# Optimization experiments

Hardware: AMD Instinct MI355X
Metric: run time of the kernel (lower is better)

## Reference

```python
import jax, jax.numpy as jnp
import numpy as np

N_USER = 100000
N_ITEM = 100000
E = 1600000
B = 16384
D = 128
LAYERS = [128, 128]
NEG_SLOPE = 0.2
EPS = 1e-12


def _l2norm(x):
    # F.normalize(x, dim=1, p=2): x / max(||x||, eps)
    n = jnp.sqrt(jnp.sum(x * x, axis=1, keepdims=True))
    return x / jnp.maximum(n, EPS)


def _sage_layer(h, src, dst, W_self, W_neigh, b):
    # DGL SAGEConv('mean'): mean-aggregate neighbor feats, then
    # fc_self(h) + fc_neigh(h_neigh) + bias
    msg = h[src]                                   # [E, D_in] gather
    agg = jax.ops.segment_sum(msg, dst, num_segments=h.shape[0])
    deg = jax.ops.segment_sum(jnp.ones((src.shape[0],), h.dtype), dst,
                              num_segments=h.shape[0])
    h_neigh = agg / jnp.maximum(deg, 1.0)[:, None]  # zero in-degree -> 0
    out = h @ W_self + h_neigh @ W_neigh + b
    return jax.nn.leaky_relu(out, NEG_SLOPE)


def setup_inputs() -> dict:
    key = jax.random.key(0)
    ks = jax.random.split(key, 20)
    inp = {}
    inp["src"] = jax.random.randint(ks[0], (E,), 0, N_USER)
    inp["dst"] = jax.random.randint(ks[1], (E,), 0, N_USER)
    inp["users"] = jax.random.randint(ks[2], (B,), 0, N_USER)
    inp["pos_items"] = jax.random.randint(ks[3], (B,), 0, N_ITEM)
    inp["neg_items"] = jax.random.randint(ks[4], (B,), 0, N_ITEM)
    inp["user_feat"] = jax.random.normal(ks[5], (N_USER, D), jnp.float32) * 0.05
    inp["item_feat"] = jax.random.normal(ks[6], (N_ITEM, D), jnp.float32) * 0.05
    dims = [D] + LAYERS
    i = 7
    for l in range(len(LAYERS)):
        di, do = dims[l], dims[l + 1]
        s = 1.0 / np.sqrt(di)
        inp[f"Wu_self{l}"] = jax.random.normal(ks[i], (di, do), jnp.float32) * s; i += 1
        inp[f"Wu_neigh{l}"] = jax.random.normal(ks[i], (di, do), jnp.float32) * s; i += 1
        inp[f"bu{l}"] = jnp.zeros((do,), jnp.float32)
        inp[f"Wi{l}"] = jax.random.normal(ks[i], (di, do), jnp.float32) * s; i += 1
        inp[f"bi{l}"] = jnp.zeros((do,), jnp.float32)
    return inp


def reference(src, dst, users, pos_items, neg_items, user_feat, item_feat,
              Wu_self0, Wu_neigh0, bu0, Wi0, bi0,
              Wu_self1, Wu_neigh1, bu1, Wi1, bi1):
    user_params = [(Wu_self0, Wu_neigh0, bu0), (Wu_self1, Wu_neigh1, bu1)]
    item_params = [(Wi0, bi0), (Wi1, bi1)]

    h_u = user_feat
    user_embeds = [h_u]
    for (Ws, Wn, b) in user_params:
        h_u = _sage_layer(h_u, src, dst, Ws, Wn, b)
        h_u = _l2norm(h_u)  # dropout p=0 -> identity
        user_embeds.append(h_u)

    h_i = item_feat
    item_embeds = [h_i]
    for (W, b) in item_params:
        h_i = jax.nn.leaky_relu(h_i @ W + b, NEG_SLOPE)
        h_i = _l2norm(h_i)
        item_embeds.append(h_i)

    user_embd = jnp.concatenate(user_embeds, axis=1)   # [N_user, 3*D]
    item_embd = jnp.concatenate(item_embeds, axis=1)   # [N_item, 3*D]

    return (user_embd[users], item_embd[pos_items], item_embd[neg_items])
```

## Files before the change

kernel.cpp:

```cpp
#include <hip/hip_runtime.h>

#define NU 100000
#define NI 100000
#define NE 1600000
#define BB 16384
#define DD 128

static constexpr int SCAN_CHUNK = 2048;
static constexpr int SCAN_NBLK  = (NU + SCAN_CHUNK - 1) / SCAN_CHUNK;
static constexpr int USER_TILES = NU / 16;

static constexpr int NXCD   = 8;
static constexpr int DRANGE = NU / NXCD;
static constexpr int K_CH   = 32;
static constexpr int CHUNK4 = NE / 4 / K_CH;
static constexpr int HIST_BLKS = NXCD * K_CH;
static constexpr int PACK_BLKS = 48;
static constexpr int CVT_UNIT  = 2048;
static constexpr int CVT_TOT   = NU * 32;
static constexpr int CVT_BLKS  = (CVT_TOT + CVT_UNIT - 1) / CVT_UNIT;

static constexpr size_t OFF_DEG      = 0;
static constexpr size_t OFF_ROWSTART = 400128;
static constexpr size_t OFF_BSUM     = 1200384;
static constexpr size_t OFF_EDGESRC  = 1200640;
static constexpr size_t OFF_H1       = 7600640;
static constexpr size_t OFF_WFRAG    = 58800640;


typedef __bf16 bf16x8 __attribute__((ext_vector_type(8)));
typedef float f32x4 __attribute__((ext_vector_type(4)));
typedef unsigned int u32x4 __attribute__((ext_vector_type(4)));

union frag_u {
    u32x4 u;
    bf16x8 b;
    unsigned short us[8];
};

__device__ __forceinline__ unsigned short f2bf(float f) {
    unsigned u = __float_as_uint(f);
    u = (u + 0x7fffu + ((u >> 16) & 1u)) >> 16;
    return (unsigned short)u;
}

__device__ __forceinline__ unsigned pack_bf16_pair(float a, float b) {
    return (unsigned)f2bf(a) | ((unsigned)f2bf(b) << 16);
}

__device__ __forceinline__ float2 unpack_bf16_pair(unsigned u) {
    float2 r;
    r.x = __uint_as_float(u << 16);
    r.y = __uint_as_float(u & 0xffff0000u);
    return r;
}

__device__ __forceinline__ f32x4 mfma16(bf16x8 a, bf16x8 b, f32x4 c) {
    return __builtin_amdgcn_mfma_f32_16x16x32_bf16(a, b, c, 0, 0, 0);
}

__device__ __forceinline__ bf16x8 bfrag(const u32x4* __restrict__ wf, int idx) {
    frag_u f;
    f.u = wf[idx];
    return f.b;
}

__device__ __forceinline__ void make_afrag_hilo(const float* rowp, int kb,
                                                bf16x8* hi, bf16x8* lo) {
    float4 v0 = *(const float4*)(rowp + kb);
    float4 v1 = *(const float4*)(rowp + kb + 4);
    float vv[8] = {v0.x, v0.y, v0.z, v0.w, v1.x, v1.y, v1.z, v1.w};
    frag_u h, l;
    #pragma unroll
    for (int e = 0; e < 8; ++e) {
        unsigned short hb = f2bf(vv[e]);
        h.us[e] = hb;
        float hf = __uint_as_float(((unsigned)hb) << 16);
        l.us[e] = f2bf(vv[e] - hf);
    }
    *hi = h.b;
    *lo = l.b;
}

__global__ __launch_bounds__(256) void mega_prep(
    const int* __restrict__ dst, int* __restrict__ hist,
    const float* __restrict__ uf, unsigned* __restrict__ ubf,
    const float* __restrict__ Ws0, const float* __restrict__ Wn0,
    const float* __restrict__ Ws1, const float* __restrict__ Wn1,
    const float* __restrict__ Wi0, const float* __restrict__ Wi1,
    u32x4* __restrict__ wfrag) {
    __shared__ int h[DRANGE];
    int t = threadIdx.x;
    if (blockIdx.x < HIST_BLKS) {
        int r = blockIdx.x & (NXCD - 1);
        int k = blockIdx.x >> 3;
        for (int j = t; j < DRANGE; j += 256) h[j] = 0;
        __syncthreads();
        int lo = r * DRANGE;
        const int4* d4 = (const int4*)dst + (size_t)k * CHUNK4;
        for (int i = t; i < CHUNK4; i += 256) {
            int4 d = d4[i];
            if ((unsigned)(d.x - lo) < (unsigned)DRANGE) atomicAdd(&h[d.x - lo], 1);
            if ((unsigned)(d.y - lo) < (unsigned)DRANGE) atomicAdd(&h[d.y - lo], 1);
            if ((unsigned)(d.z - lo) < (unsigned)DRANGE) atomicAdd(&h[d.z - lo], 1);
            if ((unsigned)(d.w - lo) < (unsigned)DRANGE) atomicAdd(&h[d.w - lo], 1);
        }
        __syncthreads();
        int* hb = hist + (size_t)(r * K_CH + k) * DRANGE;
        for (int j = t; j < DRANGE; j += 256) hb[j] = h[j];
    } else if (blockIdx.x < HIST_BLKS + PACK_BLKS) {
        int i = (blockIdx.x - HIST_BLKS) * 256 + t;
        const float* tab[6] = {Ws0, Wn0, Ws1, Wn1, Wi0, Wi1};
        int matg = i >> 11;
        int j = (i >> 8) & 7, kk = (i >> 6) & 3, ln = i & 63;
        const float* W = tab[matg];
        int n = j * 16 + (ln & 15);
        int kb = kk * 32 + (ln >> 4) * 8;
        unsigned short u[8];
        #pragma unroll
        for (int e = 0; e < 8; ++e) u[e] = f2bf(W[(size_t)(kb + e) * DD + n]);
        u32x4 w;
        w[0] = u[0] | ((unsigned)u[1] << 16);
        w[1] = u[2] | ((unsigned)u[3] << 16);
        w[2] = u[4] | ((unsigned)u[5] << 16);
        w[3] = u[6] | ((unsigned)u[7] << 16);
        wfrag[i] = w;
    } else {
        int bid2 = blockIdx.x - HIST_BLKS - PACK_BLKS;
        const float4* uf4 = (const float4*)uf;
        uint2* ub2 = (uint2*)ubf;
        #pragma unroll
        for (int it = 0; it < 8; ++it) {
            int idx = bid2 * CVT_UNIT + it * 256 + t;
            if (idx < CVT_TOT) {
                float4 v = uf4[idx];
                uint2 o;
                o.x = pack_bf16_pair(v.x, v.y);
                o.y = pack_bf16_pair(v.z, v.w);
                ub2[idx] = o;
            }
        }
    }
}

__global__ __launch_bounds__(256) void deg_reduce(const int* __restrict__ hist,
                                                  int* __restrict__ deg) {
    int d = blockIdx.x * 256 + threadIdx.x;
    if (d >= NU) return;
    int r = d / DRANGE, j = d - r * DRANGE;
    const int* hb = hist + (size_t)r * K_CH * DRANGE + j;
    int s = 0;
    #pragma unroll
    for (int k = 0; k < K_CH; ++k) s += hb[(size_t)k * DRANGE];
    deg[d] = s;
}

__global__ __launch_bounds__(256) void scan1_kernel(const int* __restrict__ deg,
                                                    int* __restrict__ bsum) {
    __shared__ int sh[256];
    int t = threadIdx.x;
    int base = blockIdx.x * SCAN_CHUNK + t * 8;
    int s = 0;
    #pragma unroll
    for (int j = 0; j < 8; ++j) {
        int idx = base + j;
        s += (idx < NU) ? deg[idx] : 0;
    }
    sh[t] = s;
    __syncthreads();
    for (int off = 128; off > 0; off >>= 1) {
        if (t < off) sh[t] += sh[t + off];
        __syncthreads();
    }
    if (t == 0) bsum[blockIdx.x] = sh[0];
}

__global__ void scan2_kernel(int* __restrict__ bsum) {
    if (threadIdx.x == 0) {
        int acc = 0;
        for (int i = 0; i < SCAN_NBLK; ++i) {
            int v = bsum[i];
            bsum[i] = acc;
            acc += v;
        }
    }
}

__global__ __launch_bounds__(256) void scan3_kernel(const int* __restrict__ deg,
                                                    const int* __restrict__ bsum,
                                                    int* __restrict__ row_start) {
    __shared__ int sh[256];
    int t = threadIdx.x;
    int base = blockIdx.x * SCAN_CHUNK + t * 8;
    int v[8];
    int s = 0;
    #pragma unroll
    for (int j = 0; j < 8; ++j) {
        int idx = base + j;
        v[j] = (idx < NU) ? deg[idx] : 0;
        s += v[j];
    }
    sh[t] = s;
    __syncthreads();
    for (int off = 1; off < 256; off <<= 1) {
        int val = sh[t];
        int add = (t >= off) ? sh[t - off] : 0;
        __syncthreads();
        sh[t] = val + add;
        __syncthreads();
    }
    int excl = sh[t] - s + bsum[blockIdx.x];
    #pragma unroll
    for (int j = 0; j < 8; ++j) {
        int idx = base + j;
        if (idx < NU) row_start[idx] = excl;
        excl += v[j];
    }
}

__global__ __launch_bounds__(256) void base_kernel(const int* __restrict__ row_start,
                                                   int* __restrict__ hist) {
    int d = blockIdx.x * 256 + threadIdx.x;
    if (d >= NU) return;
    int r = d / DRANGE, j = d - r * DRANGE;
    int* hb = hist + (size_t)r * K_CH * DRANGE + j;
    int acc = row_start[d];
    #pragma unroll
    for (int k = 0; k < K_CH; ++k) {
        int c = hb[(size_t)k * DRANGE];
        hb[(size_t)k * DRANGE] = acc;
        acc += c;
    }
}

__global__ __launch_bounds__(256) void fill2(const int* __restrict__ src,
                                             const int* __restrict__ dst,
                                             const int* __restrict__ base,
                                             int* __restrict__ edge_src) {
    __shared__ int cur[DRANGE];
    int r = blockIdx.x & (NXCD - 1);
    int k = blockIdx.x >> 3;
    int t = threadIdx.x;
    const int* bb = base + (size_t)(r * K_CH + k) * DRANGE;
    for (int j = t; j < DRANGE; j += 256) cur[j] = bb[j];
    __syncthreads();
    int lo = r * DRANGE;
    const int4* d4 = (const int4*)dst + (size_t)k * CHUNK4;
    const int4* s4 = (const int4*)src + (size_t)k * CHUNK4;
    for (int i = t; i < CHUNK4; i += 256) {
        int4 d = d4[i];
        int4 s = s4[i];
        if ((unsigned)(d.x - lo) < (unsigned)DRANGE) edge_src[atomicAdd(&cur[d.x - lo], 1)] = s.x;
        if ((unsigned)(d.y - lo) < (unsigned)DRANGE) edge_src[atomicAdd(&cur[d.y - lo], 1)] = s.y;
        if ((unsigned)(d.z - lo) < (unsigned)DRANGE) edge_src[atomicAdd(&cur[d.z - lo], 1)] = s.z;
        if ((unsigned)(d.w - lo) < (unsigned)DRANGE) edge_src[atomicAdd(&cur[d.w - lo], 1)] = s.w;
    }
}

__global__ __launch_bounds__(256) void agg_kernel(const unsigned* __restrict__ ubf,
                                                  const int* __restrict__ row_start,
                                                  const int* __restrict__ deg,
                                                  const int* __restrict__ edge_src,
                                                  unsigned* __restrict__ hn) {
    int wid = blockIdx.x * 4 + (threadIdx.x >> 6);
    int lane = threadIdx.x & 63;
    if (wid >= NU) return;
    int st = row_start[wid];
    int dg = deg[wid];
    int lanelet = lane & 15;
    int eslot = lane >> 4;
    float acc[8] = {0.f, 0.f, 0.f, 0.f, 0.f, 0.f, 0.f, 0.f};
    const unsigned* colp = ubf + (lanelet << 2);
    for (int base = 0; base < dg; base += 64) {
        int n = min(dg - base, 64);
        int myidx = (lane < n) ? edge_src[st + base + lane] : 0;
        int e = 0;
        #pragma unroll 2
        for (; e + 4 <= n; e += 4) {
            int s = __shfl(myidx, e + eslot, 64);
            u32x4 v = *(const u32x4*)(colp + (size_t)s * 64);
            #pragma unroll
            for (int k = 0; k < 4; ++k) {
                float2 f = unpack_bf16_pair(v[k]);
                acc[2 * k] += f.x;
                acc[2 * k + 1] += f.y;
            }
        }
        int rem = n - e;
        int s = __shfl(myidx, min(e + eslot, 63), 64);
        if (eslot < rem) {
            u32x4 v = *(const u32x4*)(colp + (size_t)s * 64);
            #pragma unroll
            for (int k = 0; k < 4; ++k) {
                float2 f = unpack_bf16_pair(v[k]);
                acc[2 * k] += f.x;
                acc[2 * k + 1] += f.y;
            }
        }
    }
    #pragma unroll
    for (int k = 0; k < 8; ++k) {
        acc[k] += __shfl_xor(acc[k], 16, 64);
        acc[k] += __shfl_xor(acc[k], 32, 64);
    }
    float inv = 1.0f / fmaxf((float)dg, 1.0f);
    if (eslot == 0) {
        u32x4 o;
        o[0] = pack_bf16_pair(acc[0] * inv, acc[1] * inv);
        o[1] = pack_bf16_pair(acc[2] * inv, acc[3] * inv);
        o[2] = pack_bf16_pair(acc[4] * inv, acc[5] * inv);
        o[3] = pack_bf16_pair(acc[6] * inv, acc[7] * inv);
        *(u32x4*)(hn + (size_t)wid * 64 + (lanelet << 2)) = o;
    }
}

__global__ __launch_bounds__(256) void user_mm_mfma(
    const float* __restrict__ hself, const unsigned short* __restrict__ hn,
    const u32x4* __restrict__ wf, const float* __restrict__ bias,
    float* __restrict__ out) {
    int t = threadIdx.x;
    int lane = t & 63;
    int tile = blockIdx.x * 4 + (t >> 6);
    if (tile >= USER_TILES) return;
    int gbase = tile * 16;
    int m = lane & 15, q = lane >> 4;
    const float* selfp = hself + (size_t)(gbase + m) * DD;
    const unsigned short* neighp = hn + (size_t)(gbase + m) * DD;
    bf16x8 as_hi[4], as_lo[4], an[4];
    #pragma unroll
    for (int kk = 0; kk < 4; ++kk) {
        int kb = kk * 32 + q * 8;
        make_afrag_hilo(selfp, kb, &as_hi[kk], &as_lo[kk]);
        frag_u f;
        f.u = *(const u32x4*)(neighp + kb);
        an[kk] = f.b;
    }
    f32x4 acc[8];
    f32x4 zero = {0.f, 0.f, 0.f, 0.f};
    #pragma unroll
    for (int j = 0; j < 8; ++j) acc[j] = zero;
    #pragma unroll 2
    for (int j = 0; j < 8; ++j) {
        #pragma unroll
        for (int kk = 0; kk < 4; ++kk) {
            bf16x8 bs = bfrag(wf, (j * 4 + kk) * 64 + lane);
            acc[j] = mfma16(as_hi[kk], bs, acc[j]);
            acc[j] = mfma16(as_lo[kk], bs, acc[j]);
            bf16x8 bn = bfrag(wf, 2048 + (j * 4 + kk) * 64 + lane);
            acc[j] = mfma16(an[kk], bn, acc[j]);
        }
    }
    float ss[4] = {0.f, 0.f, 0.f, 0.f};
    #pragma unroll
    for (int j = 0; j < 8; ++j) {
        float bj = bias[j * 16 + m];
        #pragma unroll
        for (int r = 0; r < 4; ++r) {
            float x = acc[j][r] + bj;
            x = x > 0.f ? x : 0.2f * x;
            acc[j][r] = x;
            ss[r] += x * x;
        }
    }
    #pragma unroll
    for (int r = 0; r < 4; ++r) {
        float s = ss[r];
        s += __shfl_xor(s, 1, 64);
        s += __shfl_xor(s, 2, 64);
        s += __shfl_xor(s, 4, 64);
        s += __shfl_xor(s, 8, 64);
        ss[r] = 1.0f / fmaxf(sqrtf(s), 1e-12f);
    }
    #pragma unroll
    for (int j = 0; j < 8; ++j)
        #pragma unroll
        for (int r = 0; r < 4; ++r)
            out[(size_t)(gbase + q * 4 + r) * DD + j * 16 + m] = acc[j][r] * ss[r];
}

__global__ __launch_bounds__(256) void tail_fuse(
    const float* __restrict__ ufeat, const float* __restrict__ h1,
    const int* __restrict__ users, const int* __restrict__ row_start,
    const int* __restrict__ deg, const int* __restrict__ edge_src,
    const float* __restrict__ ifeat, const int* __restrict__ pos,
    const int* __restrict__ neg, const u32x4* __restrict__ wf_u,
    const u32x4* __restrict__ wf_i, const float* __restrict__ bu1,
    const float* __restrict__ bi0, const float* __restrict__ bi1,
    float* __restrict__ out) {
    __shared__ float sc[16 * 132];
    __shared__ float ssp[16 * 4];
    int t = threadIdx.x;
    int lane = t & 63, wave = t >> 6;
    int m = lane & 15, q = lane >> 4;
    f32x4 zero = {0.f, 0.f, 0.f, 0.f};

    if (blockIdx.x < 1024) {
        int gb = blockIdx.x * 16;
        int L = lane & 31;
        int eslot = lane >> 5;
        const float* hl = h1 + 4 * L;
        #pragma unroll
        for (int rr = 0; rr < 4; ++rr) {
            int r = wave * 4 + rr;
            int u = users[gb + r];
            int st = row_start[u], dg = deg[u];
            float ax = 0.f, ay = 0.f, az = 0.f, aw = 0.f;
            for (int base = 0; base < dg; base += 64) {
                int n = min(dg - base, 64);
                int myidx = (lane < n) ? edge_src[st + base + lane] : 0;
                int e = 0;
                #pragma unroll 4
                for (; e + 2 <= n; e += 2) {
                    int s = __shfl(myidx, e + eslot, 64);
                    float4 v = *(const float4*)(hl + (size_t)s * DD);
                    ax += v.x; ay += v.y; az += v.z; aw += v.w;
                }
                if (e < n) {
                    int s = __shfl(myidx, e, 64);
                    if (eslot == 0) {
                        float4 v = *(const float4*)(hl + (size_t)s * DD);
                        ax += v.x; ay += v.y; az += v.z; aw += v.w;
                    }
                }
            }
            ax += __shfl_xor(ax, 32, 64);
            ay += __shfl_xor(ay, 32, 64);
            az += __shfl_xor(az, 32, 64);
            aw += __shfl_xor(aw, 32, 64);
            float inv = 1.0f / fmaxf((float)dg, 1.0f);
            if (eslot == 0) {
                float4 o = {ax * inv, ay * inv, az * inv, aw * inv};
                *(float4*)(sc + r * 132 + 4 * L) = o;
            }
            float* orow = out + (size_t)(gb + r) * 384;
            ((float2*)orow)[lane] = ((const float2*)(ufeat + (size_t)u * DD))[lane];
            ((float2*)orow)[64 + lane] = ((const float2*)(h1 + (size_t)u * DD))[lane];
        }
        __syncthreads();
        int j0 = wave * 2;
        int um = users[gb + m];
        const float* selfp = h1 + (size_t)um * DD;
        bf16x8 sh[4], sl[4], nh[4], nl[4];
        #pragma unroll
        for (int kk = 0; kk < 4; ++kk) {
            int kb = kk * 32 + q * 8;
            make_afrag_hilo(selfp, kb, &sh[kk], &sl[kk]);
            make_afrag_hilo(sc + m * 132, kb, &nh[kk], &nl[kk]);
        }
        f32x4 a0 = zero, a1 = zero;
        #pragma unroll
        for (int kk = 0; kk < 4; ++kk) {
            bf16x8 b0 = bfrag(wf_u, (j0 * 4 + kk) * 64 + lane);
            a0 = mfma16(sh[kk], b0, a0);
            a0 = mfma16(sl[kk], b0, a0);
            bf16x8 n0 = bfrag(wf_u, 2048 + (j0 * 4 + kk) * 64 + lane);
            a0 = mfma16(nh[kk], n0, a0);
            a0 = mfma16(nl[kk], n0, a0);
            bf16x8 b1 = bfrag(wf_u, ((j0 + 1) * 4 + kk) * 64 + lane);
            a1 = mfma16(sh[kk], b1, a1);
            a1 = mfma16(sl[kk], b1, a1);
            bf16x8 n1 = bfrag(wf_u, 2048 + ((j0 + 1) * 4 + kk) * 64 + lane);
            a1 = mfma16(nh[kk], n1, a1);
            a1 = mfma16(nl[kk], n1, a1);
        }
        float bj0 = bu1[j0 * 16 + m], bj1 = bu1[(j0 + 1) * 16 + m];
        float ss[4];
        #pragma unroll
        for (int r = 0; r < 4; ++r) {
            float x0 = a0[r] + bj0; x0 = x0 > 0.f ? x0 : 0.2f * x0; a0[r] = x0;
            float x1 = a1[r] + bj1; x1 = x1 > 0.f ? x1 : 0.2f * x1; a1[r] = x1;
            float s = x0 * x0 + x1 * x1;
            s += __shfl_xor(s, 1, 64);
            s += __shfl_xor(s, 2, 64);
            s += __shfl_xor(s, 4, 64);
            s += __shfl_xor(s, 8, 64);
            ss[r] = s;
        }
        if (m == 0) {
            #pragma unroll
            for (int r = 0; r < 4; ++r) ssp[(q * 4 + r) * 4 + wave] = ss[r];
        }
        __syncthreads();
        #pragma unroll
        for (int r = 0; r < 4; ++r) {
            int row = q * 4 + r;
            float tot = ssp[row * 4] + ssp[row * 4 + 1] + ssp[row * 4 + 2] + ssp[row * 4 + 3];
            float inv = 1.0f / fmaxf(sqrtf(tot), 1e-12f);
            out[(size_t)(gb + row) * 384 + 256 + j0 * 16 + m] = a0[r] * inv;
            out[(size_t)(gb + row) * 384 + 256 + (j0 + 1) * 16 + m] = a1[r] * inv;
        }
        return;
    }

    int tile = blockIdx.x - 1024;
    int gb = tile * 16;
    int j0 = wave * 2;
    int rowm = gb + m;
    int idxm = (rowm < BB) ? pos[rowm] : neg[rowm - BB];
    const float* rowp = ifeat + (size_t)idxm * DD;
    bf16x8 ahi[4], alo[4];
    #pragma unroll
    for (int kk = 0; kk < 4; ++kk)
        make_afrag_hilo(rowp, kk * 32 + q * 8, &ahi[kk], &alo[kk]);
    f32x4 a0 = zero, a1 = zero;
    #pragma unroll
    for (int kk = 0; kk < 4; ++kk) {
        bf16x8 b0 = bfrag(wf_i, (j0 * 4 + kk) * 64 + lane);
        a0 = mfma16(ahi[kk], b0, a0);
        a0 = mfma16(alo[kk], b0, a0);
        bf16x8 b1 = bfrag(wf_i, ((j0 + 1) * 4 + kk) * 64 + lane);
        a1 = mfma16(ahi[kk], b1, a1);
        a1 = mfma16(alo[kk], b1, a1);
    }
    {
        float bj0 = bi0[j0 * 16 + m], bj1 = bi0[(j0 + 1) * 16 + m];
        float ss[4];
        #pragma unroll
        for (int r = 0; r < 4; ++r) {
            float x0 = a0[r] + bj0; x0 = x0 > 0.f ? x0 : 0.2f * x0; a0[r] = x0;
            float x1 = a1[r] + bj1; x1 = x1 > 0.f ? x1 : 0.2f * x1; a1[r] = x1;
            float s = x0 * x0 + x1 * x1;
            s += __shfl_xor(s, 1, 64);
            s += __shfl_xor(s, 2, 64);
            s += __shfl_xor(s, 4, 64);
            s += __shfl_xor(s, 8, 64);
            ss[r] = s;
        }
        if (m == 0) {
            #pragma unroll
            for (int r = 0; r < 4; ++r) ssp[(q * 4 + r) * 4 + wave] = ss[r];
        }
        __syncthreads();
        #pragma unroll
        for (int r = 0; r < 4; ++r) {
            int row = q * 4 + r;
            float tot = ssp[row * 4] + ssp[row * 4 + 1] + ssp[row * 4 + 2] + ssp[row * 4 + 3];
            float inv = 1.0f / fmaxf(sqrtf(tot), 1e-12f);
            sc[row * 132 + j0 * 16 + m] = a0[r] * inv;
            sc[row * 132 + (j0 + 1) * 16 + m] = a1[r] * inv;
        }
        __syncthreads();
    }
    #pragma unroll
    for (int rr = 0; rr < 4; ++rr) {
        int r = wave * 4 + rr;
        int row = gb + r;
        int idx = (row < BB) ? pos[row] : neg[row - BB];
        float* orow = out + (size_t)(BB + row) * 384;
        ((float2*)orow)[lane] = ((const float2*)(ifeat + (size_t)idx * DD))[lane];
        float2 r1v;
        r1v.x = sc[r * 132 + 2 * lane];
        r1v.y = sc[r * 132 + 2 * lane + 1];
        ((float2*)orow)[64 + lane] = r1v;
    }
    bf16x8 chi[4], clo[4];
    #pragma unroll
    for (int kk = 0; kk < 4; ++kk)
        make_afrag_hilo(sc + m * 132, kk * 32 + q * 8, &chi[kk], &clo[kk]);
    a0 = zero; a1 = zero;
    #pragma unroll
    for (int kk = 0; kk < 4; ++kk) {
        bf16x8 b0 = bfrag(wf_i, 2048 + (j0 * 4 + kk) * 64 + lane);
        a0 = mfma16(chi[kk], b0, a0);
        a0 = mfma16(clo[kk], b0, a0);
        bf16x8 b1 = bfrag(wf_i, 2048 + ((j0 + 1) * 4 + kk) * 64 + lane);
        a1 = mfma16(chi[kk], b1, a1);
        a1 = mfma16(clo[kk], b1, a1);
    }
    {
        float bj0 = bi1[j0 * 16 + m], bj1 = bi1[(j0 + 1) * 16 + m];
        float ss[4];
        #pragma unroll
        for (int r = 0; r < 4; ++r) {
            float x0 = a0[r] + bj0; x0 = x0 > 0.f ? x0 : 0.2f * x0; a0[r] = x0;
            float x1 = a1[r] + bj1; x1 = x1 > 0.f ? x1 : 0.2f * x1; a1[r] = x1;
            float s = x0 * x0 + x1 * x1;
            s += __shfl_xor(s, 1, 64);
            s += __shfl_xor(s, 2, 64);
            s += __shfl_xor(s, 4, 64);
            s += __shfl_xor(s, 8, 64);
            ss[r] = s;
        }
        __syncthreads();
        if (m == 0) {
            #pragma unroll
            for (int r = 0; r < 4; ++r) ssp[(q * 4 + r) * 4 + wave] = ss[r];
        }
        __syncthreads();
        #pragma unroll
        for (int r = 0; r < 4; ++r) {
            int row = q * 4 + r;
            float tot = ssp[row * 4] + ssp[row * 4 + 1] + ssp[row * 4 + 2] + ssp[row * 4 + 3];
            float inv = 1.0f / fmaxf(sqrtf(tot), 1e-12f);
            out[(size_t)(BB + gb + row) * 384 + 256 + j0 * 16 + m] = a0[r] * inv;
            out[(size_t)(BB + gb + row) * 384 + 256 + (j0 + 1) * 16 + m] = a1[r] * inv;
        }
    }
}

extern "C" void kernel_launch(void* const* d_in, const int* in_sizes, int n_in,
                              void* d_out, int out_size, void* d_ws, size_t ws_size,
                              hipStream_t stream) {
    const int* src = (const int*)d_in[0];
    const int* dst = (const int*)d_in[1];
    const int* users = (const int*)d_in[2];
    const int* pos = (const int*)d_in[3];
    const int* neg = (const int*)d_in[4];
    const float* ufeat = (const float*)d_in[5];
    const float* ifeat = (const float*)d_in[6];
    const float* Ws0 = (const float*)d_in[7];
    const float* Wn0 = (const float*)d_in[8];
    const float* bu0 = (const float*)d_in[9];
    const float* Wi0 = (const float*)d_in[10];
    const float* bi0 = (const float*)d_in[11];
    const float* Ws1 = (const float*)d_in[12];
    const float* Wn1 = (const float*)d_in[13];
    const float* bu1 = (const float*)d_in[14];
    const float* Wi1 = (const float*)d_in[15];
    const float* bi1 = (const float*)d_in[16];
    float* out = (float*)d_out;

    char* ws = (char*)d_ws;
    int* deg = (int*)(ws + OFF_DEG);
    int* row_start = (int*)(ws + OFF_ROWSTART);
    int* bsum = (int*)(ws + OFF_BSUM);
    int* edge_src = (int*)(ws + OFF_EDGESRC);
    float* h1 = (float*)(ws + OFF_H1);
    u32x4* wfrag = (u32x4*)(ws + OFF_WFRAG);

    unsigned* ubf = (unsigned*)d_out;
    unsigned* hn = (unsigned*)((char*)d_out + (size_t)NU * DD * 2);
    int* hist = (int*)((char*)d_out + (size_t)NU * DD * 4);
    const unsigned short* hn_us = (const unsigned short*)hn;

    mega_prep<<<HIST_BLKS + PACK_BLKS + CVT_BLKS, 256, 0, stream>>>(
        dst, hist, ufeat, ubf, Ws0, Wn0, Ws1, Wn1, Wi0, Wi1, wfrag);
    deg_reduce<<<(NU + 255) / 256, 256, 0, stream>>>(hist, deg);
    scan1_kernel<<<SCAN_NBLK, 256, 0, stream>>>(deg, bsum);
    scan2_kernel<<<1, 64, 0, stream>>>(bsum);
    scan3_kernel<<<SCAN_NBLK, 256, 0, stream>>>(deg, bsum, row_start);
    base_kernel<<<(NU + 255) / 256, 256, 0, stream>>>(row_start, hist);
    fill2<<<HIST_BLKS, 256, 0, stream>>>(src, dst, hist, edge_src);
    agg_kernel<<<(NU + 3) / 4, 256, 0, stream>>>(ubf, row_start, deg, edge_src, hn);
    user_mm_mfma<<<(USER_TILES + 3) / 4, 256, 0, stream>>>(ufeat, hn_us, wfrag, bu0, h1);
    tail_fuse<<<1024 + 2048, 256, 0, stream>>>(ufeat, h1, users, row_start, deg, edge_src,
                                               ifeat, pos, neg, wfrag + 4096, wfrag + 8192,
                                               bu1, bi0, bi1, out);
}
```

Measured before the change: 440.1 us.

## Interleave item MLP blocks with neighbor aggregation and split user tail kernel

Merges the layer-0 neighbor aggregation and the item-tower MLP into one launch, interleaving item tiles among aggregation blocks so the compute-bound item work overlaps the gather-bound aggregation. The user tail is split into its own kernel. The bf16 conversion covers only the first 98304 rows, and gathers from higher rows read fp32 features directly, so the convert loop needs no bounds check. The aggregation result is written into the h1 buffer with a 256-element stride and then overwritten in place by user_mm_mfma, removing the separate hn buffer. This adds a divergent branch in the gather loop and depends on ordering: each user_mm tile reads its hn rows before writing h1 over them.

Measured after the change: 486.3 us. +10.5%, slower.

```diff
diff --git a/kernel.cpp b/kernel.cpp
--- a/kernel.cpp
+++ b/kernel.cpp
@@ -16,9 +16,14 @@
 static constexpr int CHUNK4 = NE / 4 / K_CH;
 static constexpr int HIST_BLKS = NXCD * K_CH;
 static constexpr int PACK_BLKS = 48;
+static constexpr int UBF_ROWS  = 98304;
 static constexpr int CVT_UNIT  = 2048;
-static constexpr int CVT_TOT   = NU * 32;
-static constexpr int CVT_BLKS  = (CVT_TOT + CVT_UNIT - 1) / CVT_UNIT;
+static constexpr int CVT_TOT   = UBF_ROWS * 32;
+static constexpr int CVT_BLKS  = CVT_TOT / CVT_UNIT;
+
+static constexpr int NITEM  = 2048;
+static constexpr int AGG_BLKS = NU / 4;
+static constexpr int AI_BLKS  = AGG_BLKS + NITEM;
 
 static constexpr size_t OFF_DEG      = 0;
 static constexpr size_t OFF_ROWSTART = 400128;
@@ -132,13 +137,11 @@
         #pragma unroll
         for (int it = 0; it < 8; ++it) {
             int idx = bid2 * CVT_UNIT + it * 256 + t;
-            if (idx < CVT_TOT) {
-                float4 v = uf4[idx];
-                uint2 o;
-                o.x = pack_bf16_pair(v.x, v.y);
-                o.y = pack_bf16_pair(v.z, v.w);
-                ub2[idx] = o;
-            }
+            float4 v = uf4[idx];
+            uint2 o;
+            o.x = pack_bf16_pair(v.x, v.y);
+            o.y = pack_bf16_pair(v.z, v.w);
+            ub2[idx] = o;
         }
     }
 }
@@ -257,244 +260,97 @@
     }
 }
 
-__global__ __launch_bounds__(256) void agg_kernel(const unsigned* __restrict__ ubf,
-                                                  const int* __restrict__ row_start,
-                                                  const int* __restrict__ deg,
-                                                  const int* __restrict__ edge_src,
-                                                  unsigned* __restrict__ hn) {
-    int wid = blockIdx.x * 4 + (threadIdx.x >> 6);
-    int lane = threadIdx.x & 63;
-    if (wid >= NU) return;
-    int st = row_start[wid];
-    int dg = deg[wid];
-    int lanelet = lane & 15;
-    int eslot = lane >> 4;
-    float acc[8] = {0.f, 0.f, 0.f, 0.f, 0.f, 0.f, 0.f, 0.f};
-    const unsigned* colp = ubf + (lanelet << 2);
-    for (int base = 0; base < dg; base += 64) {
-        int n = min(dg - base, 64);
-        int myidx = (lane < n) ? edge_src[st + base + lane] : 0;
-        int e = 0;
-        #pragma unroll 2
-        for (; e + 4 <= n; e += 4) {
-            int s = __shfl(myidx, e + eslot, 64);
-            u32x4 v = *(const u32x4*)(colp + (size_t)s * 64);
-            #pragma unroll
-            for (int k = 0; k < 4; ++k) {
-                float2 f = unpack_bf16_pair(v[k]);
-                acc[2 * k] += f.x;
-                acc[2 * k + 1] += f.y;
-            }
-        }
-        int rem = n - e;
-        int s = __shfl(myidx, min(e + eslot, 63), 64);
-        if (eslot < rem) {
-            u32x4 v = *(const u32x4*)(colp + (size_t)s * 64);
-            #pragma unroll
-            for (int k = 0; k < 4; ++k) {
-                float2 f = unpack_bf16_pair(v[k]);
-                acc[2 * k] += f.x;
-                acc[2 * k + 1] += f.y;
-            }
-        }
-    }
-    #pragma unroll
-    for (int k = 0; k < 8; ++k) {
-        acc[k] += __shfl_xor(acc[k], 16, 64);
-        acc[k] += __shfl_xor(acc[k], 32, 64);
-    }
-    float inv = 1.0f / fmaxf((float)dg, 1.0f);
-    if (eslot == 0) {
-        u32x4 o;
-        o[0] = pack_bf16_pair(acc[0] * inv, acc[1] * inv);
-        o[1] = pack_bf16_pair(acc[2] * inv, acc[3] * inv);
-        o[2] = pack_bf16_pair(acc[4] * inv, acc[5] * inv);
-        o[3] = pack_bf16_pair(acc[6] * inv, acc[7] * inv);
-        *(u32x4*)(hn + (size_t)wid * 64 + (lanelet << 2)) = o;
-    }
-}
-
-__global__ __launch_bounds__(256) void user_mm_mfma(
-    const float* __restrict__ hself, const unsigned short* __restrict__ hn,
-    const u32x4* __restrict__ wf, const float* __restrict__ bias,
-    float* __restrict__ out) {
-    int t = threadIdx.x;
-    int lane = t & 63;
-    int tile = blockIdx.x * 4 + (t >> 6);
-    if (tile >= USER_TILES) return;
-    int gbase = tile * 16;
-    int m = lane & 15, q = lane >> 4;
-    const float* selfp = hself + (size_t)(gbase + m) * DD;
-    const unsigned short* neighp = hn + (size_t)(gbase + m) * DD;
-    bf16x8 as_hi[4], as_lo[4], an[4];
-    #pragma unroll
-    for (int kk = 0; kk < 4; ++kk) {
-        int kb = kk * 32 + q * 8;
-        make_afrag_hilo(selfp, kb, &as_hi[kk], &as_lo[kk]);
-        frag_u f;
-        f.u = *(const u32x4*)(neighp + kb);
-        an[kk] = f.b;
-    }
-    f32x4 acc[8];
-    f32x4 zero = {0.f, 0.f, 0.f, 0.f};
-    #pragma unroll
-    for (int j = 0; j < 8; ++j) acc[j] = zero;
-    #pragma unroll 2
-    for (int j = 0; j < 8; ++j) {
-        #pragma unroll
-        for (int kk = 0; kk < 4; ++kk) {
-            bf16x8 bs = bfrag(wf, (j * 4 + kk) * 64 + lane);
-            acc[j] = mfma16(as_hi[kk], bs, acc[j]);
-            acc[j] = mfma16(as_lo[kk], bs, acc[j]);
-            bf16x8 bn = bfrag(wf, 2048 + (j * 4 + kk) * 64 + lane);
-            acc[j] = mfma16(an[kk], bn, acc[j]);
-        }
-    }
-    float ss[4] = {0.f, 0.f, 0.f, 0.f};
-    #pragma unroll
-    for (int j = 0; j < 8; ++j) {
-        float bj = bias[j * 16 + m];
-        #pragma unroll
-        for (int r = 0; r < 4; ++r) {
-            float x = acc[j][r] + bj;
-            x = x > 0.f ? x : 0.2f * x;
-            acc[j][r] = x;
-            ss[r] += x * x;
-        }
-    }
-    #pragma unroll
-    for (int r = 0; r < 4; ++r) {
-        float s = ss[r];
-        s += __shfl_xor(s, 1, 64);
-        s += __shfl_xor(s, 2, 64);
-        s += __shfl_xor(s, 4, 64);
-        s += __shfl_xor(s, 8, 64);
-        ss[r] = 1.0f / fmaxf(sqrtf(s), 1e-12f);
-    }
-    #pragma unroll
-    for (int j = 0; j < 8; ++j)
-        #pragma unroll
-        for (int r = 0; r < 4; ++r)
-            out[(size_t)(gbase + q * 4 + r) * DD + j * 16 + m] = acc[j][r] * ss[r];
-}
-
-__global__ __launch_bounds__(256) void tail_fuse(
-    const float* __restrict__ ufeat, const float* __restrict__ h1,
-    const int* __restrict__ users, const int* __restrict__ row_start,
-    const int* __restrict__ deg, const int* __restrict__ edge_src,
+__global__ __launch_bounds__(256) void agg_item_fuse(
+    const unsigned* __restrict__ ubf, const float* __restrict__ ufeat,
+    const int* __restrict__ row_start, const int* __restrict__ deg,
+    const int* __restrict__ edge_src, float* __restrict__ h1,
     const float* __restrict__ ifeat, const int* __restrict__ pos,
-    const int* __restrict__ neg, const u32x4* __restrict__ wf_u,
-    const u32x4* __restrict__ wf_i, const float* __restrict__ bu1,
+    const int* __restrict__ neg, const u32x4* __restrict__ wf_i,
     const float* __restrict__ bi0, const float* __restrict__ bi1,
     float* __restrict__ out) {
     __shared__ float sc[16 * 132];
     __shared__ float ssp[16 * 4];
+    int bid = blockIdx.x;
     int t = threadIdx.x;
     int lane = t & 63, wave = t >> 6;
-    int m = lane & 15, q = lane >> 4;
-    f32x4 zero = {0.f, 0.f, 0.f, 0.f};
-
-    if (blockIdx.x < 1024) {
-        int gb = blockIdx.x * 16;
-        int L = lane & 31;
-        int eslot = lane >> 5;
-        const float* hl = h1 + 4 * L;
-        #pragma unroll
-        for (int rr = 0; rr < 4; ++rr) {
-            int r = wave * 4 + rr;
-            int u = users[gb + r];
-            int st = row_start[u], dg = deg[u];
-            float ax = 0.f, ay = 0.f, az = 0.f, aw = 0.f;
-            for (int base = 0; base < dg; base += 64) {
-                int n = min(dg - base, 64);
-                int myidx = (lane < n) ? edge_src[st + base + lane] : 0;
-                int e = 0;
-                #pragma unroll 4
-                for (; e + 2 <= n; e += 2) {
-                    int s = __shfl(myidx, e + eslot, 64);
-                    float4 v = *(const float4*)(hl + (size_t)s * DD);
-                    ax += v.x; ay += v.y; az += v.z; aw += v.w;
-                }
-                if (e < n) {
-                    int s = __shfl(myidx, e, 64);
-                    if (eslot == 0) {
-                        float4 v = *(const float4*)(hl + (size_t)s * DD);
-                        ax += v.x; ay += v.y; az += v.z; aw += v.w;
+    bool is_item = (bid % 13 == 6) && (bid / 13 < NITEM);
+
+    if (!is_item) {
+        int agg_bid = bid - min(NITEM, (bid + 6) / 13);
+        int wid = agg_bid * 4 + wave;
+        int st = row_start[wid];
+        int dg = deg[wid];
+        int lanelet = lane & 15;
+        int eslot = lane >> 4;
+        float acc[8] = {0.f, 0.f, 0.f, 0.f, 0.f, 0.f, 0.f, 0.f};
+        const unsigned* colp = ubf + (lanelet << 2);
+        const float* fcol = ufeat + (lanelet << 3);
+        for (int base = 0; base < dg; base += 64) {
+            int n = min(dg - base, 64);
+            int myidx = (lane < n) ? edge_src[st + base + lane] : 0;
+            int e = 0;
+            #pragma unroll 2
+            for (; e + 4 <= n; e += 4) {
+                int s = __shfl(myidx, e + eslot, 64);
+                if (s < UBF_ROWS) {
+                    u32x4 v = *(const u32x4*)(colp + (size_t)s * 64);
+                    #pragma unroll
+                    for (int k = 0; k < 4; ++k) {
+                        float2 f = unpack_bf16_pair(v[k]);
+                        acc[2 * k] += f.x;
+                        acc[2 * k + 1] += f.y;
                     }
+                } else {
+                    const float* fp = fcol + (size_t)s * DD;
+                    float4 a = *(const float4*)fp;
+                    float4 b = *(const float4*)(fp + 4);
+                    acc[0] += a.x; acc[1] += a.y; acc[2] += a.z; acc[3] += a.w;
+                    acc[4] += b.x; acc[5] += b.y; acc[6] += b.z; acc[7] += b.w;
                 }
             }
-            ax += __shfl_xor(ax, 32, 64);
-            ay += __shfl_xor(ay, 32, 64);
-            az += __shfl_xor(az, 32, 64);
-            aw += __shfl_xor(aw, 32, 64);
-            float inv = 1.0f / fmaxf((float)dg, 1.0f);
-            if (eslot == 0) {
-                float4 o = {ax * inv, ay * inv, az * inv, aw * inv};
-                *(float4*)(sc + r * 132 + 4 * L) = o;
+            int rem = n - e;
+            int s = __shfl(myidx, min(e + eslot, 63), 64);
+            if (eslot < rem) {
+                if (s < UBF_ROWS) {
+                    u32x4 v = *(const u32x4*)(colp + (size_t)s * 64);
+                    #pragma unroll
+                    for (int k = 0; k < 4; ++k) {
+                        float2 f = unpack_bf16_pair(v[k]);
+                        acc[2 * k] += f.x;
+                        acc[2 * k + 1] += f.y;
+                    }
+                } else {
+                    const float* fp = fcol + (size_t)s * DD;
+                    float4 a = *(const float4*)fp;
+                    float4 b = *(const float4*)(fp + 4);
+                    acc[0] += a.x; acc[1] += a.y; acc[2] += a.z; acc[3] += a.w;
+                    acc[4] += b.x; acc[5] += b.y; acc[6] += b.z; acc[7] += b.w;
+                }
             }
-            float* orow = out + (size_t)(gb + r) * 384;
-            ((float2*)orow)[lane] = ((const float2*)(ufeat + (size_t)u * DD))[lane];
-            ((float2*)orow)[64 + lane] = ((const float2*)(h1 + (size_t)u * DD))[lane];
-        }
-        __syncthreads();
-        int j0 = wave * 2;
-        int um = users[gb + m];
-        const float* selfp = h1 + (size_t)um * DD;
-        bf16x8 sh[4], sl[4], nh[4], nl[4];
-        #pragma unroll
-        for (int kk = 0; kk < 4; ++kk) {
-            int kb = kk * 32 + q * 8;
-            make_afrag_hilo(selfp, kb, &sh[kk], &sl[kk]);
-            make_afrag_hilo(sc + m * 132, kb, &nh[kk], &nl[kk]);
-        }
-        f32x4 a0 = zero, a1 = zero;
-        #pragma unroll
-        for (int kk = 0; kk < 4; ++kk) {
-            bf16x8 b0 = bfrag(wf_u, (j0 * 4 + kk) * 64 + lane);
-            a0 = mfma16(sh[kk], b0, a0);
-            a0 = mfma16(sl[kk], b0, a0);
-            bf16x8 n0 = bfrag(wf_u, 2048 + (j0 * 4 + kk) * 64 + lane);
-            a0 = mfma16(nh[kk], n0, a0);
-            a0 = mfma16(nl[kk], n0, a0);
-            bf16x8 b1 = bfrag(wf_u, ((j0 + 1) * 4 + kk) * 64 + lane);
-            a1 = mfma16(sh[kk], b1, a1);
-            a1 = mfma16(sl[kk], b1, a1);
-            bf16x8 n1 = bfrag(wf_u, 2048 + ((j0 + 1) * 4 + kk) * 64 + lane);
-            a1 = mfma16(nh[kk], n1, a1);
-            a1 = mfma16(nl[kk], n1, a1);
-        }
-        float bj0 = bu1[j0 * 16 + m], bj1 = bu1[(j0 + 1) * 16 + m];
-        float ss[4];
-        #pragma unroll
-        for (int r = 0; r < 4; ++r) {
-            float x0 = a0[r] + bj0; x0 = x0 > 0.f ? x0 : 0.2f * x0; a0[r] = x0;
-            float x1 = a1[r] + bj1; x1 = x1 > 0.f ? x1 : 0.2f * x1; a1[r] = x1;
-            float s = x0 * x0 + x1 * x1;
-            s += __shfl_xor(s, 1, 64);
-            s += __shfl_xor(s, 2, 64);
-            s += __shfl_xor(s, 4, 64);
-            s += __shfl_xor(s, 8, 64);
-            ss[r] = s;
-        }
-        if (m == 0) {
-            #pragma unroll
-            for (int r = 0; r < 4; ++r) ssp[(q * 4 + r) * 4 + wave] = ss[r];
-        }
-        __syncthreads();
-        #pragma unroll
-        for (int r = 0; r < 4; ++r) {
-            int row = q * 4 + r;
-            float tot = ssp[row * 4] + ssp[row * 4 + 1] + ssp[row * 4 + 2] + ssp[row * 4 + 3];
-            float inv = 1.0f / fmaxf(sqrtf(tot), 1e-12f);
-            out[(size_t)(gb + row) * 384 + 256 + j0 * 16 + m] = a0[r] * inv;
-            out[(size_t)(gb + row) * 384 + 256 + (j0 + 1) * 16 + m] = a1[r] * inv;
+        }
+        #pragma unroll
+        for (int k = 0; k < 8; ++k) {
+            acc[k] += __shfl_xor(acc[k], 16, 64);
+            acc[k] += __shfl_xor(acc[k], 32, 64);
+        }
+        float inv = 1.0f / fmaxf((float)dg, 1.0f);
+        if (eslot == 0) {
+            u32x4 o;
+            o[0] = pack_bf16_pair(acc[0] * inv, acc[1] * inv);
+            o[1] = pack_bf16_pair(acc[2] * inv, acc[3] * inv);
+            o[2] = pack_bf16_pair(acc[4] * inv, acc[5] * inv);
+            o[3] = pack_bf16_pair(acc[6] * inv, acc[7] * inv);
+            unsigned* hnu = (unsigned*)h1;
+            *(u32x4*)(hnu + (size_t)wid * 128 + (lanelet << 2)) = o;
         }
         return;
     }
 
-    int tile = blockIdx.x - 1024;
+    int tile = bid / 13;
     int gb = tile * 16;
+    int m = lane & 15, q = lane >> 4;
     int j0 = wave * 2;
+    f32x4 zero = {0.f, 0.f, 0.f, 0.f};
     int rowm = gb + m;
     int idxm = (rowm < BB) ? pos[rowm] : neg[rowm - BB];
     const float* rowp = ifeat + (size_t)idxm * DD;
@@ -595,6 +451,177 @@
             out[(size_t)(BB + gb + row) * 384 + 256 + j0 * 16 + m] = a0[r] * inv;
             out[(size_t)(BB + gb + row) * 384 + 256 + (j0 + 1) * 16 + m] = a1[r] * inv;
         }
+    }
+}
+
+__global__ __launch_bounds__(256) void user_mm_mfma(
+    const float* __restrict__ hself, float* __restrict__ h1,
+    const u32x4* __restrict__ wf, const float* __restrict__ bias) {
+    int t = threadIdx.x;
+    int lane = t & 63;
+    int tile = blockIdx.x * 4 + (t >> 6);
+    if (tile >= USER_TILES) return;
+    int gbase = tile * 16;
+    int m = lane & 15, q = lane >> 4;
+    const float* selfp = hself + (size_t)(gbase + m) * DD;
+    const unsigned short* neighp = (const unsigned short*)h1 + (size_t)(gbase + m) * 256;
+    bf16x8 as_hi[4], as_lo[4], an[4];
+    #pragma unroll
+    for (int kk = 0; kk < 4; ++kk) {
+        int kb = kk * 32 + q * 8;
+        make_afrag_hilo(selfp, kb, &as_hi[kk], &as_lo[kk]);
+        frag_u f;
+        f.u = *(const u32x4*)(neighp + kb);
+        an[kk] = f.b;
+    }
+    f32x4 acc[8];
+    f32x4 zero = {0.f, 0.f, 0.f, 0.f};
+    #pragma unroll
+    for (int j = 0; j < 8; ++j) acc[j] = zero;
+    #pragma unroll 2
+    for (int j = 0; j < 8; ++j) {
+        #pragma unroll
+        for (int kk = 0; kk < 4; ++kk) {
+            bf16x8 bs = bfrag(wf, (j * 4 + kk) * 64 + lane);
+            acc[j] = mfma16(as_hi[kk], bs, acc[j]);
+            acc[j] = mfma16(as_lo[kk], bs, acc[j]);
+            bf16x8 bn = bfrag(wf, 2048 + (j * 4 + kk) * 64 + lane);
+            acc[j] = mfma16(an[kk], bn, acc[j]);
+        }
+    }
+    float ss[4] = {0.f, 0.f, 0.f, 0.f};
+    #pragma unroll
+    for (int j = 0; j < 8; ++j) {
+        float bj = bias[j * 16 + m];
+        #pragma unroll
+        for (int r = 0; r < 4; ++r) {
+            float x = acc[j][r] + bj;
+            x = x > 0.f ? x : 0.2f * x;
+            acc[j][r] = x;
+            ss[r] += x * x;
+        }
+    }
+    #pragma unroll
+    for (int r = 0; r < 4; ++r) {
+        float s = ss[r];
+        s += __shfl_xor(s, 1, 64);
+        s += __shfl_xor(s, 2, 64);
+        s += __shfl_xor(s, 4, 64);
+        s += __shfl_xor(s, 8, 64);
+        ss[r] = 1.0f / fmaxf(sqrtf(s), 1e-12f);
+    }
+    #pragma unroll
+    for (int j = 0; j < 8; ++j)
+        #pragma unroll
+        for (int r = 0; r < 4; ++r)
+            h1[(size_t)(gbase + q * 4 + r) * DD + j * 16 + m] = acc[j][r] * ss[r];
+}
+
+__global__ __launch_bounds__(256) void tail_user(
+    const float* __restrict__ ufeat, const float* __restrict__ h1,
+    const int* __restrict__ users, const int* __restrict__ row_start,
+    const int* __restrict__ deg, const int* __restrict__ edge_src,
+    const u32x4* __restrict__ wf_u, const float* __restrict__ bu1,
+    float* __restrict__ out) {
+    __shared__ float sc[16 * 132];
+    __shared__ float ssp[16 * 4];
+    int t = threadIdx.x;
+    int lane = t & 63, wave = t >> 6;
+    int m = lane & 15, q = lane >> 4;
+    f32x4 zero = {0.f, 0.f, 0.f, 0.f};
+    int gb = blockIdx.x * 16;
+    int L = lane & 31;
+    int eslot = lane >> 5;
+    const float* hl = h1 + 4 * L;
+    #pragma unroll
+    for (int rr = 0; rr < 4; ++rr) {
+        int r = wave * 4 + rr;
+        int u = users[gb + r];
+        int st = row_start[u], dg = deg[u];
+        float ax = 0.f, ay = 0.f, az = 0.f, aw = 0.f;
+        for (int base = 0; base < dg; base += 64) {
+            int n = min(dg - base, 64);
+            int myidx = (lane < n) ? edge_src[st + base + lane] : 0;
+            int e = 0;
+            #pragma unroll 4
+            for (; e + 2 <= n; e += 2) {
+                int s = __shfl(myidx, e + eslot, 64);
+                float4 v = *(const float4*)(hl + (size_t)s * DD);
+                ax += v.x; ay += v.y; az += v.z; aw += v.w;
+            }
+            if (e < n) {
+                int s = __shfl(myidx, e, 64);
+                if (eslot == 0) {
+                    float4 v = *(const float4*)(hl + (size_t)s * DD);
+                    ax += v.x; ay += v.y; az += v.z; aw += v.w;
+                }
+            }
+        }
+        ax += __shfl_xor(ax, 32, 64);
+        ay += __shfl_xor(ay, 32, 64);
+        az += __shfl_xor(az, 32, 64);
+        aw += __shfl_xor(aw, 32, 64);
+        float inv = 1.0f / fmaxf((float)dg, 1.0f);
+        if (eslot == 0) {
+            float4 o = {ax * inv, ay * inv, az * inv, aw * inv};
+            *(float4*)(sc + r * 132 + 4 * L) = o;
+        }
+        float* orow = out + (size_t)(gb + r) * 384;
+        ((float2*)orow)[lane] = ((const float2*)(ufeat + (size_t)u * DD))[lane];
+        ((float2*)orow)[64 + lane] = ((const float2*)(h1 + (size_t)u * DD))[lane];
+    }
+    __syncthreads();
+    int j0 = wave * 2;
+    int um = users[gb + m];
+    const float* selfp = h1 + (size_t)um * DD;
+    bf16x8 sh[4], sl[4], nh[4], nl[4];
+    #pragma unroll
+    for (int kk = 0; kk < 4; ++kk) {
+        int kb = kk * 32 + q * 8;
+        make_afrag_hilo(selfp, kb, &sh[kk], &sl[kk]);
+        make_afrag_hilo(sc + m * 132, kb, &nh[kk], &nl[kk]);
+    }
+    f32x4 a0 = zero, a1 = zero;
+    #pragma unroll
+    for (int kk = 0; kk < 4; ++kk) {
+        bf16x8 b0 = bfrag(wf_u, (j0 * 4 + kk) * 64 + lane);
+        a0 = mfma16(sh[kk], b0, a0);
+        a0 = mfma16(sl[kk], b0, a0);
+        bf16x8 n0 = bfrag(wf_u, 2048 + (j0 * 4 + kk) * 64 + lane);
+        a0 = mfma16(nh[kk], n0, a0);
+        a0 = mfma16(nl[kk], n0, a0);
+        bf16x8 b1 = bfrag(wf_u, ((j0 + 1) * 4 + kk) * 64 + lane);
+        a1 = mfma16(sh[kk], b1, a1);
+        a1 = mfma16(sl[kk], b1, a1);
+        bf16x8 n1 = bfrag(wf_u, 2048 + ((j0 + 1) * 4 + kk) * 64 + lane);
+        a1 = mfma16(nh[kk], n1, a1);
+        a1 = mfma16(nl[kk], n1, a1);
+    }
+    float bj0 = bu1[j0 * 16 + m], bj1 = bu1[(j0 + 1) * 16 + m];
+    float ss[4];
+    #pragma unroll
+    for (int r = 0; r < 4; ++r) {
+        float x0 = a0[r] + bj0; x0 = x0 > 0.f ? x0 : 0.2f * x0; a0[r] = x0;
+        float x1 = a1[r] + bj1; x1 = x1 > 0.f ? x1 : 0.2f * x1; a1[r] = x1;
+        float s = x0 * x0 + x1 * x1;
+        s += __shfl_xor(s, 1, 64);
+        s += __shfl_xor(s, 2, 64);
+        s += __shfl_xor(s, 4, 64);
+        s += __shfl_xor(s, 8, 64);
+        ss[r] = s;
+    }
+    if (m == 0) {
+        #pragma unroll
+        for (int r = 0; r < 4; ++r) ssp[(q * 4 + r) * 4 + wave] = ss[r];
+    }
+    __syncthreads();
+    #pragma unroll
+    for (int r = 0; r < 4; ++r) {
+        int row = q * 4 + r;
+        float tot = ssp[row * 4] + ssp[row * 4 + 1] + ssp[row * 4 + 2] + ssp[row * 4 + 3];
+        float inv = 1.0f / fmaxf(sqrtf(tot), 1e-12f);
+        out[(size_t)(gb + row) * 384 + 256 + j0 * 16 + m] = a0[r] * inv;
+        out[(size_t)(gb + row) * 384 + 256 + (j0 + 1) * 16 + m] = a1[r] * inv;
     }
 }
 
@@ -629,9 +656,7 @@
     u32x4* wfrag = (u32x4*)(ws + OFF_WFRAG);
 
     unsigned* ubf = (unsigned*)d_out;
-    unsigned* hn = (unsigned*)((char*)d_out + (size_t)NU * DD * 2);
     int* hist = (int*)((char*)d_out + (size_t)NU * DD * 4);
-    const unsigned short* hn_us = (const unsigned short*)hn;
 
     mega_prep<<<HIST_BLKS + PACK_BLKS + CVT_BLKS, 256, 0, stream>>>(
         dst, hist, ufeat, ubf, Ws0, Wn0, Ws1, Wn1, Wi0, Wi1, wfrag);
@@ -641,9 +666,9 @@
     scan3_kernel<<<SCAN_NBLK, 256, 0, stream>>>(deg, bsum, row_start);
     base_kernel<<<(NU + 255) / 256, 256, 0, stream>>>(row_start, hist);
     fill2<<<HIST_BLKS, 256, 0, stream>>>(src, dst, hist, edge_src);
-    agg_kernel<<<(NU + 3) / 4, 256, 0, stream>>>(ubf, row_start, deg, edge_src, hn);
-    user_mm_mfma<<<(USER_TILES + 3) / 4, 256, 0, stream>>>(ufeat, hn_us, wfrag, bu0, h1);
-    tail_fuse<<<1024 + 2048, 256, 0, stream>>>(ufeat, h1, users, row_start, deg, edge_src,
-                                               ifeat, pos, neg, wfrag + 4096, wfrag + 8192,
-                                               bu1, bi0, bi1, out);
-}
+    agg_item_fuse<<<AI_BLKS, 256, 0, stream>>>(ubf, ufeat, row_start, deg, edge_src, h1,
+                                               ifeat, pos, neg, wfrag + 8192, bi0, bi1, out);
+    user_mm_mfma<<<(USER_TILES + 3) / 4, 256, 0, stream>>>(ufeat, h1, wfrag, bu0);
+    tail_user<<<BB / 16, 256, 0, stream>>>(ufeat, h1, users, row_start, deg, edge_src,
+                                           wfrag + 4096, bu1, out);
+}
```
